# Kernel optimization log

Measured on AMD Instinct MI355X. Metric: run time of the kernel, lower is better.

The kernel has to match this reference:

```python
import jax, jax.numpy as jnp
import numpy as np

EPS = 1e-6

def _normalize(A):
    # zero the diagonal, add self-loops
    n = A.shape[-1]
    eye = jnp.eye(n, dtype=A.dtype)
    A_hat = A * (1.0 - eye) + eye  # [B,N,N]
    # symmetric degree normalization with eps inside as in the TF code:
    # d = 1/(eps + sqrt(rowsum)); norm = diag(d) @ A_hat @ diag(d)
    d = 1.0 / (EPS + jnp.sqrt(jnp.sum(A_hat, axis=2)))  # [B,N]
    return A_hat * d[:, :, None] * d[:, None, :]


def setup_inputs() -> dict:
    key = jax.random.key(0)
    k1, k2, k3 = jax.random.split(key, 3)
    B, N, F, O = 8, 2048, 128, 128
    x = jax.random.normal(k1, (B, N, F), dtype=jnp.float32)
    adj = jax.random.uniform(k2, (B, N, N), dtype=jnp.float32)
    kernel = jax.random.normal(k3, (F, O), dtype=jnp.float32) * 0.05
    return {"x": x, "adj": adj, "kernel": kernel}


def reference(x, adj, kernel):
    norm = _normalize(adj)                      # [B,N,N]
    agg = jnp.einsum('bnm,bmf->bnf', norm, x)   # batch_dot
    out = jnp.einsum('bnf,fo->bno', agg, kernel)
    return jax.nn.relu(out)
```

## Files before the change

### kernel.cpp

```cpp
#include <hip/hip_runtime.h>


typedef __bf16 bf16x8 __attribute__((ext_vector_type(8)));
typedef __bf16 bf16x4 __attribute__((ext_vector_type(4)));
typedef float  f32x4  __attribute__((ext_vector_type(4)));

#define NN 2048
#define NB 8

__global__ __launch_bounds__(256) void wt_kernel(const float* __restrict__ W,
                                                 __bf16* __restrict__ Wt) {
    int idx = blockIdx.x * 256 + threadIdx.x;
    int f = idx >> 7, o = idx & 127;
    Wt[o * 128 + f] = (__bf16)W[idx];
}

__global__ __launch_bounds__(256) void prep_kernel(const float* __restrict__ adj,
                                                   float* __restrict__ dvec,
                                                   __bf16* __restrict__ adjb) {
    const int lane = threadIdx.x & 63;
    const int row  = blockIdx.x * 4 + (threadIdx.x >> 6);
    const float* rp = adj + (size_t)row * NN;
    __bf16* wp = adjb + (size_t)row * NN;
    const int n = row & (NN - 1);

    f32x4 v[8];
    float s = 0.f;
#pragma unroll
    for (int it = 0; it < 8; ++it) {
        v[it] = *(const f32x4*)(rp + it * 256 + lane * 4);
        s += (v[it].x + v[it].y) + (v[it].z + v[it].w);
    }
#pragma unroll
    for (int off = 1; off < 64; off <<= 1) s += __shfl_xor(s, off);
    float diag = rp[n];
    float d = 1.0f / (1e-6f + sqrtf(s - diag + 1.0f));
    if (lane == 0) dvec[row] = d;

#pragma unroll
    for (int it = 0; it < 8; ++it) {
        int c0 = it * 256 + lane * 4;
        float f0 = (c0     == n) ? 1.0f : v[it].x;
        float f1 = (c0 + 1 == n) ? 1.0f : v[it].y;
        float f2 = (c0 + 2 == n) ? 1.0f : v[it].z;
        float f3 = (c0 + 3 == n) ? 1.0f : v[it].w;
        bf16x4 o4;
        o4[0] = (__bf16)(f0 * d); o4[1] = (__bf16)(f1 * d);
        o4[2] = (__bf16)(f2 * d); o4[3] = (__bf16)(f3 * d);
        *(bf16x4*)(wp + c0) = o4;
    }
}

__global__ __launch_bounds__(256) void xw_kernel(const float* __restrict__ x,
                                                 const __bf16* __restrict__ Wt,
                                                 const float* __restrict__ dvec,
                                                 __bf16* __restrict__ yt) {
    const int lane = threadIdx.x & 63;
    const int wave = threadIdx.x >> 6;
    const int b    = blockIdx.x & 7;
    const int mt   = (blockIdx.x >> 3) * 4 + wave;
    const int m0   = mt * 16;
    const int kgrp = (lane >> 4) * 8;
    const float* xp = x + ((size_t)b * NN + m0 + (lane & 15)) * 128 + kgrp;

    f32x4 acc[8];
#pragma unroll
    for (int i = 0; i < 8; ++i) acc[i] = (f32x4){0.f, 0.f, 0.f, 0.f};

#pragma unroll
    for (int kt = 0; kt < 4; ++kt) {
        f32x4 a0 = *(const f32x4*)(xp + kt * 32);
        f32x4 a1 = *(const f32x4*)(xp + kt * 32 + 4);
        float av[8] = {a0.x, a0.y, a0.z, a0.w, a1.x, a1.y, a1.z, a1.w};
        bf16x8 af;
#pragma unroll
        for (int j = 0; j < 8; ++j) af[j] = (__bf16)av[j];
#pragma unroll
        for (int nb = 0; nb < 8; ++nb) {
            bf16x8 bfv = *(const bf16x8*)(Wt + (nb * 16 + (lane & 15)) * 128 +
                                          kt * 32 + kgrp);
            acc[nb] = __builtin_amdgcn_mfma_f32_16x16x32_bf16(af, bfv, acc[nb], 0, 0, 0);
        }
    }
    const int col0 = lane & 15;
    const int rq   = (lane >> 4) * 4;
#pragma unroll
    for (int r = 0; r < 4; ++r) {
        int m = m0 + rq + r;
        float dm = dvec[b * NN + m];
#pragma unroll
        for (int nb = 0; nb < 8; ++nb) {
            int o = nb * 16 + col0;
            yt[((size_t)b * 128 + o) * NN + m] = (__bf16)(acc[nb][r] * dm);
        }
    }
}

__global__ __launch_bounds__(256) void gemm_kernel(const __bf16* __restrict__ adjb,
                                                   const __bf16* __restrict__ yt,
                                                   float* __restrict__ out) {
    const int lane = threadIdx.x & 63;
    const int wave = threadIdx.x >> 6;
    const int b    = blockIdx.x & 7;
    const int tile = blockIdx.x >> 3;
    const int rsel = (wave & 1) * 16;
    const int csel = (wave >> 1) * 64;
    const int kgrp = (lane >> 4) * 8;

    const __bf16* ap =
        adjb + ((size_t)b * NN + tile * 32 + rsel + (lane & 15)) * NN + kgrp;
    const __bf16* bbase = yt + (size_t)b * 128 * NN + kgrp;
    const __bf16* bp0 = bbase + (size_t)(csel + 0 * 16 + (lane & 15)) * NN;
    const __bf16* bp1 = bbase + (size_t)(csel + 1 * 16 + (lane & 15)) * NN;
    const __bf16* bp2 = bbase + (size_t)(csel + 2 * 16 + (lane & 15)) * NN;
    const __bf16* bp3 = bbase + (size_t)(csel + 3 * 16 + (lane & 15)) * NN;

    f32x4 acc[4];
#pragma unroll
    for (int i = 0; i < 4; ++i) acc[i] = (f32x4){0.f, 0.f, 0.f, 0.f};

#pragma unroll 4
    for (int kt = 0; kt < 64; ++kt) {
        const int ko = kt * 32;
        bf16x8 af  = *(const bf16x8*)(ap  + ko);
        bf16x8 bf0 = *(const bf16x8*)(bp0 + ko);
        bf16x8 bf1 = *(const bf16x8*)(bp1 + ko);
        bf16x8 bf2 = *(const bf16x8*)(bp2 + ko);
        bf16x8 bf3 = *(const bf16x8*)(bp3 + ko);
        acc[0] = __builtin_amdgcn_mfma_f32_16x16x32_bf16(af, bf0, acc[0], 0, 0, 0);
        acc[1] = __builtin_amdgcn_mfma_f32_16x16x32_bf16(af, bf1, acc[1], 0, 0, 0);
        acc[2] = __builtin_amdgcn_mfma_f32_16x16x32_bf16(af, bf2, acc[2], 0, 0, 0);
        acc[3] = __builtin_amdgcn_mfma_f32_16x16x32_bf16(af, bf3, acc[3], 0, 0, 0);
    }

    const int col0 = lane & 15;
    const int rq   = (lane >> 4) * 4;
    float* op = out + ((size_t)b * NN + tile * 32 + rsel) * 128;
#pragma unroll
    for (int r = 0; r < 4; ++r) {
#pragma unroll
        for (int nb = 0; nb < 4; ++nb) {
            float v = acc[nb][r];
            op[(rq + r) * 128 + csel + nb * 16 + col0] = v > 0.f ? v : 0.f;
        }
    }
}

extern "C" void kernel_launch(void* const* d_in, const int* in_sizes, int n_in,
                              void* d_out, int out_size, void* d_ws, size_t ws_size,
                              hipStream_t stream) {
    const float* x   = (const float*)d_in[0];
    const float* adj = (const float*)d_in[1];
    const float* W   = (const float*)d_in[2];
    float* out = (float*)d_out;

    char* ws = (char*)d_ws;
    float*  dvec = (float*)ws;
    __bf16* Wt   = (__bf16*)(ws + (64 << 10));
    __bf16* yt   = (__bf16*)(ws + (128 << 10));
    __bf16* adjb = (__bf16*)(ws + (128 << 10) + ((size_t)NB * 128 * NN * 2));

    hipLaunchKernelGGL(wt_kernel, dim3(64), dim3(256), 0, stream, W, Wt);
    hipLaunchKernelGGL(prep_kernel, dim3(NB * NN / 4), dim3(256), 0, stream,
                       adj, dvec, adjb);
    hipLaunchKernelGGL(xw_kernel, dim3(256), dim3(256), 0, stream,
                       x, Wt, dvec, yt);
    hipLaunchKernelGGL(gemm_kernel, dim3(512), dim3(256), 0, stream,
                       adjb, yt, out);
}
```

Before: 288.7 us.

## Drop bf16 adjacency copy; GEMM reads fp32 adj directly with LDS-staged B

The prep kernel no longer writes a normalized bf16 copy of adj. It only computes the degree vector. The GEMM now loads raw fp32 adj, converts it to bf16 in registers, and applies the diagonal fix and row scaling in the epilogue with a correction term. B tiles are staged into double-buffered LDS through global_load_lds, and A is prefetched one step ahead. This avoids writing and re-reading a 64MB intermediate, but the GEMM now reads twice as many bytes of A and adds a barrier every k-step.

```diff
diff --git a/kernel.cpp b/kernel.cpp
--- a/kernel.cpp
+++ b/kernel.cpp
@@ -8,6 +8,12 @@
 #define NN 2048
 #define NB 8
 
+__device__ __forceinline__ void load_lds16(__bf16* lds, const __bf16* g) {
+    __builtin_amdgcn_global_load_lds(
+        (const __attribute__((address_space(1))) void*)g,
+        (__attribute__((address_space(3))) void*)lds, 16, 0, 0);
+}
+
 __global__ __launch_bounds__(256) void wt_kernel(const float* __restrict__ W,
                                                  __bf16* __restrict__ Wt) {
     int idx = blockIdx.x * 256 + threadIdx.x;
@@ -15,39 +21,24 @@
     Wt[o * 128 + f] = (__bf16)W[idx];
 }
 
-__global__ __launch_bounds__(256) void prep_kernel(const float* __restrict__ adj,
-                                                   float* __restrict__ dvec,
-                                                   __bf16* __restrict__ adjb) {
+__global__ __launch_bounds__(256) void d_kernel(const float* __restrict__ adj,
+                                                float* __restrict__ dvec) {
     const int lane = threadIdx.x & 63;
     const int row  = blockIdx.x * 4 + (threadIdx.x >> 6);
     const float* rp = adj + (size_t)row * NN;
-    __bf16* wp = adjb + (size_t)row * NN;
-    const int n = row & (NN - 1);
-
-    f32x4 v[8];
-    float s = 0.f;
+    float4 s4 = {0.f, 0.f, 0.f, 0.f};
 #pragma unroll
     for (int it = 0; it < 8; ++it) {
-        v[it] = *(const f32x4*)(rp + it * 256 + lane * 4);
-        s += (v[it].x + v[it].y) + (v[it].z + v[it].w);
+        float4 v = *(const float4*)(rp + it * 256 + lane * 4);
+        s4.x += v.x; s4.y += v.y; s4.z += v.z; s4.w += v.w;
     }
+    float s = (s4.x + s4.y) + (s4.z + s4.w);
 #pragma unroll
-    for (int off = 1; off < 64; off <<= 1) s += __shfl_xor(s, off);
-    float diag = rp[n];
-    float d = 1.0f / (1e-6f + sqrtf(s - diag + 1.0f));
-    if (lane == 0) dvec[row] = d;
-
-#pragma unroll
-    for (int it = 0; it < 8; ++it) {
-        int c0 = it * 256 + lane * 4;
-        float f0 = (c0     == n) ? 1.0f : v[it].x;
-        float f1 = (c0 + 1 == n) ? 1.0f : v[it].y;
-        float f2 = (c0 + 2 == n) ? 1.0f : v[it].z;
-        float f3 = (c0 + 3 == n) ? 1.0f : v[it].w;
-        bf16x4 o4;
-        o4[0] = (__bf16)(f0 * d); o4[1] = (__bf16)(f1 * d);
-        o4[2] = (__bf16)(f2 * d); o4[3] = (__bf16)(f3 * d);
-        *(bf16x4*)(wp + c0) = o4;
+    for (int off = 32; off; off >>= 1) s += __shfl_down(s, off);
+    if (lane == 0) {
+        int n = row & (NN - 1);
+        float sh = s - rp[n] + 1.0f;
+        dvec[row] = 1.0f / (1e-6f + sqrtf(sh));
     }
 }
 
@@ -96,52 +87,79 @@
     }
 }
 
-__global__ __launch_bounds__(256) void gemm_kernel(const __bf16* __restrict__ adjb,
+__global__ __launch_bounds__(256) void gemm_kernel(const float* __restrict__ adj,
                                                    const __bf16* __restrict__ yt,
+                                                   const float* __restrict__ dvec,
                                                    float* __restrict__ out) {
-    const int lane = threadIdx.x & 63;
-    const int wave = threadIdx.x >> 6;
+    __shared__ alignas(16) __bf16 sB[2][128][32];
+
+    const int tid  = threadIdx.x;
+    const int wave = tid >> 6;
+    const int lane = tid & 63;
     const int b    = blockIdx.x & 7;
     const int tile = blockIdx.x >> 3;
     const int rsel = (wave & 1) * 16;
     const int csel = (wave >> 1) * 64;
     const int kgrp = (lane >> 4) * 8;
 
-    const __bf16* ap =
-        adjb + ((size_t)b * NN + tile * 32 + rsel + (lane & 15)) * NN + kgrp;
-    const __bf16* bbase = yt + (size_t)b * 128 * NN + kgrp;
-    const __bf16* bp0 = bbase + (size_t)(csel + 0 * 16 + (lane & 15)) * NN;
-    const __bf16* bp1 = bbase + (size_t)(csel + 1 * 16 + (lane & 15)) * NN;
-    const __bf16* bp2 = bbase + (size_t)(csel + 2 * 16 + (lane & 15)) * NN;
-    const __bf16* bp3 = bbase + (size_t)(csel + 3 * 16 + (lane & 15)) * NN;
+    const int arow_loc = tile * 32 + rsel + (lane & 15);
+    const float* ap = adj + ((size_t)b * NN + arow_loc) * NN + kgrp;
+
+    const __bf16* ytb = yt + (size_t)b * 128 * NN;
+    const int b_row0 = wave * 32;
+    const __bf16* b_src = ytb + (size_t)(b_row0 + (lane >> 2)) * NN + (lane & 3) * 8;
 
     f32x4 acc[4];
 #pragma unroll
     for (int i = 0; i < 4; ++i) acc[i] = (f32x4){0.f, 0.f, 0.f, 0.f};
 
-#pragma unroll 4
+    load_lds16(&sB[0][b_row0][0], b_src);
+    load_lds16(&sB[0][b_row0 + 16][0], b_src + (size_t)16 * NN);
+    f32x4 ca0 = *(const f32x4*)(ap);
+    f32x4 ca1 = *(const f32x4*)(ap + 4);
+
     for (int kt = 0; kt < 64; ++kt) {
-        const int ko = kt * 32;
-        bf16x8 af  = *(const bf16x8*)(ap  + ko);
-        bf16x8 bf0 = *(const bf16x8*)(bp0 + ko);
-        bf16x8 bf1 = *(const bf16x8*)(bp1 + ko);
-        bf16x8 bf2 = *(const bf16x8*)(bp2 + ko);
-        bf16x8 bf3 = *(const bf16x8*)(bp3 + ko);
-        acc[0] = __builtin_amdgcn_mfma_f32_16x16x32_bf16(af, bf0, acc[0], 0, 0, 0);
-        acc[1] = __builtin_amdgcn_mfma_f32_16x16x32_bf16(af, bf1, acc[1], 0, 0, 0);
-        acc[2] = __builtin_amdgcn_mfma_f32_16x16x32_bf16(af, bf2, acc[2], 0, 0, 0);
-        acc[3] = __builtin_amdgcn_mfma_f32_16x16x32_bf16(af, bf3, acc[3], 0, 0, 0);
+        const int cur = kt & 1;
+        __syncthreads();
+
+        f32x4 na0, na1;
+        if (kt + 1 < 64) {
+            const __bf16* bs = b_src + (size_t)(kt + 1) * 32;
+            load_lds16(&sB[cur ^ 1][b_row0][0], bs);
+            load_lds16(&sB[cur ^ 1][b_row0 + 16][0], bs + (size_t)16 * NN);
+            na0 = *(const f32x4*)(ap + (kt + 1) * 32);
+            na1 = *(const f32x4*)(ap + (kt + 1) * 32 + 4);
+        }
+
+        bf16x8 af;
+        af[0] = (__bf16)ca0.x; af[1] = (__bf16)ca0.y;
+        af[2] = (__bf16)ca0.z; af[3] = (__bf16)ca0.w;
+        af[4] = (__bf16)ca1.x; af[5] = (__bf16)ca1.y;
+        af[6] = (__bf16)ca1.z; af[7] = (__bf16)ca1.w;
+
+#pragma unroll
+        for (int nb = 0; nb < 4; ++nb) {
+            bf16x8 bfv = *(const bf16x8*)(
+                &sB[cur][csel + nb * 16 + (lane & 15)][kgrp]);
+            acc[nb] = __builtin_amdgcn_mfma_f32_16x16x32_bf16(af, bfv, acc[nb], 0, 0, 0);
+        }
+        ca0 = na0; ca1 = na1;
     }
 
     const int col0 = lane & 15;
     const int rq   = (lane >> 4) * 4;
-    float* op = out + ((size_t)b * NN + tile * 32 + rsel) * 128;
 #pragma unroll
     for (int r = 0; r < 4; ++r) {
+        int n_loc = tile * 32 + rsel + rq + r;
+        size_t grow = (size_t)b * NN + n_loc;
+        float dn   = dvec[grow];
+        float cfac = 1.0f - adj[grow * NN + n_loc];
 #pragma unroll
         for (int nb = 0; nb < 4; ++nb) {
-            float v = acc[nb][r];
-            op[(rq + r) * 128 + csel + nb * 16 + col0] = v > 0.f ? v : 0.f;
+            int o = csel + nb * 16 + col0;
+            float yp = (float)ytb[(size_t)o * NN + n_loc];
+            float v = (acc[nb][r] + cfac * yp) * dn;
+            out[grow * 128 + o] = v > 0.f ? v : 0.f;
         }
     }
 }
@@ -158,13 +176,10 @@
     float*  dvec = (float*)ws;
     __bf16* Wt   = (__bf16*)(ws + (64 << 10));
     __bf16* yt   = (__bf16*)(ws + (128 << 10));
-    __bf16* adjb = (__bf16*)(ws + (128 << 10) + ((size_t)NB * 128 * NN * 2));
 
     hipLaunchKernelGGL(wt_kernel, dim3(64), dim3(256), 0, stream, W, Wt);
-    hipLaunchKernelGGL(prep_kernel, dim3(NB * NN / 4), dim3(256), 0, stream,
-                       adj, dvec, adjb);
-    hipLaunchKernelGGL(xw_kernel, dim3(256), dim3(256), 0, stream,
-                       x, Wt, dvec, yt);
+    hipLaunchKernelGGL(d_kernel, dim3(NB * NN / 4), dim3(256), 0, stream, adj, dvec);
+    hipLaunchKernelGGL(xw_kernel, dim3(256), dim3(256), 0, stream, x, Wt, dvec, yt);
     hipLaunchKernelGGL(gemm_kernel, dim3(512), dim3(256), 0, stream,
-                       adjb, yt, out);
+                       adj, yt, dvec, out);
 }
```

After: 248.2 us. 1.16x faster.
